# Optimization experiments

Measured on AMD Instinct MI355X. Metric: run time of the kernel, lower is better.

The kernel has to match this reference:

```python
import jax, jax.numpy as jnp
import numpy as np

N, NFEAT, NHID, NCLASS, NHEADS = 50000, 512, 256, 64, 8
C1 = NHID // NHEADS  # 32 per-head channels, layer 1
NEG_SLOPE = 0.2


def setup_inputs() -> dict:
    key = jax.random.key(0)
    ks = jax.random.split(key, 10)
    x = jax.random.normal(ks[0], (N, NFEAT), dtype=jnp.float32)
    edge_idx = jax.random.randint(ks[1], (2, 800000), 0, N, dtype=jnp.int64)
    s = 0.05
    return {
        "x": x,
        "edge_idx": edge_idx,
        "W1": jax.random.normal(ks[2], (NFEAT, NHEADS, C1), dtype=jnp.float32) * s,
        "a1_src": jax.random.normal(ks[3], (NHEADS, C1), dtype=jnp.float32) * s,
        "a1_dst": jax.random.normal(ks[4], (NHEADS, C1), dtype=jnp.float32) * s,
        "b1": jnp.zeros((NHID,), dtype=jnp.float32),
        "W2": jax.random.normal(ks[5], (NHID, NHEADS, NCLASS), dtype=jnp.float32) * s,
        "a2_src": jax.random.normal(ks[6], (NHEADS, NCLASS), dtype=jnp.float32) * s,
        "a2_dst": jax.random.normal(ks[7], (NHEADS, NCLASS), dtype=jnp.float32) * s,
        "b2": jnp.zeros((NCLASS,), dtype=jnp.float32),
    }


def gat_conv(x, src, dst, W, a_src, a_dst, b, concat):
    # x: [N, F_in]; W: [F_in, H, C]; a_*: [H, C]; src/dst: [E]
    h = jnp.einsum("nf,fhc->nhc", x, W)             # [N, H, C]
    e_src = jnp.sum(h * a_src, axis=-1)              # [N, H]
    e_dst = jnp.sum(h * a_dst, axis=-1)              # [N, H]
    alpha = e_src[src] + e_dst[dst]                  # [E, H]
    alpha = jnp.where(alpha > 0, alpha, NEG_SLOPE * alpha)  # leaky_relu(0.2)
    # segment softmax over incoming edges of each destination node
    m = jax.ops.segment_max(alpha, dst, num_segments=N)     # [N, H]
    m = jnp.where(jnp.isfinite(m), m, 0.0)
    e = jnp.exp(alpha - m[dst])                      # [E, H]
    z = jax.ops.segment_sum(e, dst, num_segments=N)  # [N, H]
    coef = e / z[dst]                                # [E, H]
    msg = h[src] * coef[:, :, None]                  # [E, H, C]
    out = jax.ops.segment_sum(msg, dst, num_segments=N)  # [N, H, C]
    if concat:
        out = out.reshape(N, -1)
    else:
        out = out.mean(axis=1)
    return out + b


def reference(x, edge_idx, W1, a1_src, a1_dst, b1, W2, a2_src, a2_dst, b2):
    # add self loops (PyG GATConv default)
    loop = jnp.arange(N, dtype=edge_idx.dtype)
    src = jnp.concatenate([edge_idx[0], loop])
    dst = jnp.concatenate([edge_idx[1], loop])
    h = gat_conv(x, src, dst, W1, a1_src, a1_dst, b1, concat=True)   # [N, NHID]
    h = jax.nn.relu(h)
    # dropout inactive (eval mode)
    out = gat_conv(h, src, dst, W2, a2_src, a2_dst, b2, concat=False)  # [N, NCLASS]
    return jax.nn.log_softmax(out, axis=1)
```

## Files before the change

kernel.cpp:

```cpp
#include <hip/hip_runtime.h>
#include <math.h>

#define NN 50000
#define NF 512
#define NHID 256
#define NCLASS 64
#define NHEADS 8

typedef __attribute__((ext_vector_type(8))) short bf16x8;
typedef __attribute__((ext_vector_type(4))) float f32x4;

static __device__ __forceinline__ unsigned short f2bf(float f) {
  unsigned int u = __float_as_uint(f);
  unsigned int r = (u + 0x7fffu + ((u >> 16) & 1u)) >> 16;
  return (unsigned short)r;
}
static __device__ __forceinline__ float bf2f(unsigned short u) {
  return __uint_as_float(((unsigned int)u) << 16);
}
static __device__ __forceinline__ float2 bfpair(unsigned int u) {
  return make_float2(__uint_as_float(u << 16), __uint_as_float(u & 0xffff0000u));
}

__global__ void k_init_deg(int* deg) {
  int i = blockIdx.x * blockDim.x + threadIdx.x;
  if (i < NN) deg[i] = 1;
}

__global__ void k_count(const int* __restrict__ dst, int E0, int* deg) {
  int i = blockIdx.x * blockDim.x + threadIdx.x;
  if (i < E0) atomicAdd(&deg[dst[i]], 1);
}

__global__ __launch_bounds__(1024) void k_scan(const int* __restrict__ deg, int* offs,
                                               int* cursor) {
  __shared__ int wbase[16];
  __shared__ int srun;
  int tid = threadIdx.x;
  int lane = tid & 63;
  int wv = tid >> 6;
  if (tid == 0) srun = 0;
  __syncthreads();
  for (int base = 0; base < NN; base += 4096) {
    int i = base + tid * 4;
    int4 v;
    if (i + 3 < NN) {
      v = *(const int4*)(deg + i);
    } else {
      v.x = (i + 0 < NN) ? deg[i + 0] : 0;
      v.y = (i + 1 < NN) ? deg[i + 1] : 0;
      v.z = (i + 2 < NN) ? deg[i + 2] : 0;
      v.w = (i + 3 < NN) ? deg[i + 3] : 0;
    }
    int tot = v.x + v.y + v.z + v.w;
    int s = tot;
    #pragma unroll
    for (int o = 1; o < 64; o <<= 1) {
      int t = __shfl_up(s, o);
      if (lane >= o) s += t;
    }
    if (lane == 63) wbase[wv] = s;
    __syncthreads();
    if (tid == 0) {
      int run = srun;
      #pragma unroll
      for (int w2 = 0; w2 < 16; w2++) {
        int t = wbase[w2];
        wbase[w2] = run;
        run += t;
      }
      srun = run;
    }
    __syncthreads();
    int p = wbase[wv] + s - tot;
    if (i + 0 < NN) { offs[i + 0] = p; cursor[i + 0] = p; p += v.x; }
    if (i + 1 < NN) { offs[i + 1] = p; cursor[i + 1] = p; p += v.y; }
    if (i + 2 < NN) { offs[i + 2] = p; cursor[i + 2] = p; p += v.z; }
    if (i + 3 < NN) { offs[i + 3] = p; cursor[i + 3] = p; }
  }
  __syncthreads();
  if (tid == 0) offs[NN] = srun;
}

__global__ void k_scatter(const int* __restrict__ src, const int* __restrict__ dst,
                          int E0, int* cursor, int* __restrict__ nbr) {
  int i = blockIdx.x * blockDim.x + threadIdx.x;
  if (i < E0) {
    int pos = atomicAdd(&cursor[dst[i]], 1);
    nbr[pos] = src[i];
  } else if (i < E0 + NN) {
    int v = i - E0;
    int pos = atomicAdd(&cursor[v], 1);
    nbr[pos] = v;
  }
}

__global__ void k_cast4(const float* __restrict__ in, unsigned short* __restrict__ out,
                        int n4) {
  int i = blockIdx.x * blockDim.x + threadIdx.x;
  if (i >= n4) return;
  float4 v = *(const float4*)(in + (size_t)i * 4);
  ushort4 o;
  o.x = f2bf(v.x); o.y = f2bf(v.y); o.z = f2bf(v.z); o.w = f2bf(v.w);
  *(ushort4*)(out + (size_t)i * 4) = o;
}

__global__ void k_castWt(const float* __restrict__ W, unsigned short* __restrict__ Wt,
                         int K, int cols) {
  int i = blockIdx.x * blockDim.x + threadIdx.x;
  if (i >= K * cols) return;
  int k = i / cols, c = i % cols;
  Wt[(size_t)c * K + k] = f2bf(W[i]);
}

__global__ void k_castWt_perm(const float* __restrict__ W, unsigned short* __restrict__ Wt,
                              int K) {
  int i = blockIdx.x * blockDim.x + threadIdx.x;
  if (i >= K * NHEADS * NCLASS) return;
  int k = i / (NHEADS * NCLASS);
  int rem = i % (NHEADS * NCLASS);
  int h = rem / NCLASS, c = rem % NCLASS;
  Wt[(size_t)(c * NHEADS + h) * K + k] = f2bf(W[i]);
}

__global__ __launch_bounds__(256) void k_gemm_bf(const unsigned short* __restrict__ A,
                                                 const unsigned short* __restrict__ Bt,
                                                 unsigned short* __restrict__ C,
                                                 int rows, int K, int cols) {
  __shared__ unsigned short Bs[256 * 40];
  int t = threadIdx.x;
  int wave = t >> 6, lane = t & 63;
  int quad = lane >> 4, sixt = lane & 15;
  int rb = blockIdx.x * 64 + (wave >> 1) * 32;
  int cw = (wave & 1) * 128;
  int cbw = blockIdx.y * 256 + cw;
  int r0 = rb + sixt, r1 = rb + 16 + sixt;
  const unsigned short* Ap0 = A + (size_t)(r0 < rows ? r0 : 0) * K + quad * 8;
  const unsigned short* Ap1 = A + (size_t)(r1 < rows ? r1 : 0) * K + quad * 8;
  const unsigned short* Bg = Bt + (size_t)(blockIdx.y * 256 + (t >> 2)) * K + (t & 3) * 8;
  const size_t BgStep = (size_t)64 * K;
  char* BsW = (char*)Bs + (t >> 2) * 80 + (t & 3) * 16;
  f32x4 acc0[8] = {}, acc1[8] = {};
  for (int k0 = 0; k0 < K; k0 += 32) {
    uint4 v0 = *(const uint4*)(Bg + k0);
    uint4 v1 = *(const uint4*)(Bg + BgStep + k0);
    uint4 v2 = *(const uint4*)(Bg + 2 * BgStep + k0);
    uint4 v3 = *(const uint4*)(Bg + 3 * BgStep + k0);
    bf16x8 a0 = *(const bf16x8*)(Ap0 + k0);
    bf16x8 a1 = *(const bf16x8*)(Ap1 + k0);
    *(uint4*)(BsW) = v0;
    *(uint4*)(BsW + 64 * 80) = v1;
    *(uint4*)(BsW + 128 * 80) = v2;
    *(uint4*)(BsW + 192 * 80) = v3;
    __syncthreads();
    #pragma unroll
    for (int g = 0; g < 8; g++) {
      bf16x8 b = *(const bf16x8*)((const char*)Bs + (cw + g * 16 + sixt) * 80 + quad * 16);
      acc0[g] = __builtin_amdgcn_mfma_f32_16x16x32_bf16(a0, b, acc0[g], 0, 0, 0);
      acc1[g] = __builtin_amdgcn_mfma_f32_16x16x32_bf16(a1, b, acc1[g], 0, 0, 0);
    }
    __syncthreads();
  }
  #pragma unroll
  for (int r = 0; r < 4; r++) {
    int row = rb + quad * 4 + r;
    if (row < rows) {
      unsigned short* out = C + (size_t)row * cols + cbw + sixt;
      #pragma unroll
      for (int g = 0; g < 8; g++) out[g * 16] = f2bf(acc0[g][r]);
    }
    int row2 = row + 16;
    if (row2 < rows) {
      unsigned short* out = C + (size_t)row2 * cols + cbw + sixt;
      #pragma unroll
      for (int g = 0; g < 8; g++) out[g * 16] = f2bf(acc1[g][r]);
    }
  }
}

template <int C>
__global__ void k_escore_c(const unsigned short* __restrict__ h,
                           const float* __restrict__ asr, const float* __restrict__ ads,
                           float* __restrict__ es, float* __restrict__ ed) {
  int idx = blockIdx.x * blockDim.x + threadIdx.x;
  if (idx >= NN * NHEADS) return;
  int hd = idx & 7;
  const unsigned short* row = h + (size_t)idx * C;
  float s = 0.f, d = 0.f;
  #pragma unroll
  for (int c8 = 0; c8 < C / 8; c8++) {
    uint4 raw = *(const uint4*)(row + c8 * 8);
    float2 p0 = bfpair(raw.x), p1 = bfpair(raw.y), p2 = bfpair(raw.z), p3 = bfpair(raw.w);
    const float* as_ = asr + hd * C + c8 * 8;
    const float* ad_ = ads + hd * C + c8 * 8;
    s += p0.x * as_[0] + p0.y * as_[1] + p1.x * as_[2] + p1.y * as_[3] +
         p2.x * as_[4] + p2.y * as_[5] + p3.x * as_[6] + p3.y * as_[7];
    d += p0.x * ad_[0] + p0.y * ad_[1] + p1.x * ad_[2] + p1.y * ad_[3] +
         p2.x * ad_[4] + p2.y * ad_[5] + p3.x * ad_[6] + p3.y * ad_[7];
  }
  es[idx] = s;
  ed[idx] = d;
}

__global__ void k_escore_p(const unsigned short* __restrict__ h,
                           const float* __restrict__ asr, const float* __restrict__ ads,
                           float* __restrict__ es, float* __restrict__ ed) {
  int idx = blockIdx.x * blockDim.x + threadIdx.x;
  if (idx >= NN * NHEADS) return;
  int hd = idx & 7;
  int n = idx >> 3;
  const unsigned short* row = h + (size_t)n * (NHEADS * NCLASS) + hd;
  float s = 0.f, d = 0.f;
  #pragma unroll
  for (int c = 0; c < NCLASS; c++) {
    float v = bf2f(row[c * NHEADS]);
    s += v * asr[hd * NCLASS + c];
    d += v * ads[hd * NCLASS + c];
  }
  es[idx] = s;
  ed[idx] = d;
}

__global__ __launch_bounds__(256) void k_agg1f(const int* __restrict__ offs,
                                               const int* __restrict__ nbr,
                                               const unsigned short* __restrict__ h1,
                                               const float* __restrict__ es,
                                               const float* __restrict__ ed,
                                               const float* __restrict__ b1,
                                               unsigned short* __restrict__ out) {
  int node = blockIdx.x * 4 + (threadIdx.x >> 6);
  if (node >= NN) return;
  int lane = threadIdx.x & 63;
  int h = lane & 7;
  int beg = offs[node], end = offs[node + 1];
  float edst = ed[node * NHEADS + h];
  float m = -1e30f, z = 0.f;
  for (int k = beg + (lane >> 3); k < end; k += 8) {
    int s = nbr[k];
    float a = es[s * NHEADS + h] + edst;
    a = (a > 0.f) ? a : 0.2f * a;
    float mn = fmaxf(m, a);
    z = z * __expf(m - mn) + __expf(a - mn);
    m = mn;
  }
  #pragma unroll
  for (int o = 8; o < 64; o <<= 1) {
    float m2 = __shfl_xor(m, o);
    float z2 = __shfl_xor(z, o);
    float mn = fmaxf(m, m2);
    z = z * __expf(m - mn) + z2 * __expf(m2 - mn);
    m = mn;
  }
  float inv = 1.f / z;
  int head = lane >> 3;
  float mh = __shfl(m, head);
  float ivh = __shfl(inv, head);
  float edh = __shfl(edst, head);
  float4 acc = make_float4(0.f, 0.f, 0.f, 0.f);
  int k = beg;
  for (; k + 1 < end; k += 2) {
    int s0 = nbr[k], s1 = nbr[k + 1];
    float a0 = es[s0 * NHEADS + head] + edh;
    float a1c = es[s1 * NHEADS + head] + edh;
    a0 = (a0 > 0.f) ? a0 : 0.2f * a0;
    a1c = (a1c > 0.f) ? a1c : 0.2f * a1c;
    float c0 = __expf(a0 - mh) * ivh;
    float c1 = __expf(a1c - mh) * ivh;
    uint2 r0 = *(const uint2*)(h1 + (size_t)s0 * NHID + (lane << 2));
    uint2 r1 = *(const uint2*)(h1 + (size_t)s1 * NHID + (lane << 2));
    float2 p0 = bfpair(r0.x), p1 = bfpair(r0.y);
    float2 q0 = bfpair(r1.x), q1 = bfpair(r1.y);
    acc.x += c0 * p0.x + c1 * q0.x;
    acc.y += c0 * p0.y + c1 * q0.y;
    acc.z += c0 * p1.x + c1 * q1.x;
    acc.w += c0 * p1.y + c1 * q1.y;
  }
  if (k < end) {
    int s0 = nbr[k];
    float a0 = es[s0 * NHEADS + head] + edh;
    a0 = (a0 > 0.f) ? a0 : 0.2f * a0;
    float c0 = __expf(a0 - mh) * ivh;
    uint2 r0 = *(const uint2*)(h1 + (size_t)s0 * NHID + (lane << 2));
    float2 p0 = bfpair(r0.x), p1 = bfpair(r0.y);
    acc.x += c0 * p0.x;
    acc.y += c0 * p0.y;
    acc.z += c0 * p1.x;
    acc.w += c0 * p1.y;
  }
  int col = lane << 2;
  ushort4 o;
  o.x = f2bf(fmaxf(acc.x + b1[col + 0], 0.f));
  o.y = f2bf(fmaxf(acc.y + b1[col + 1], 0.f));
  o.z = f2bf(fmaxf(acc.z + b1[col + 2], 0.f));
  o.w = f2bf(fmaxf(acc.w + b1[col + 3], 0.f));
  *(ushort4*)(out + (size_t)node * NHID + col) = o;
}

__global__ __launch_bounds__(256) void k_agg2f(const int* __restrict__ offs,
                                               const int* __restrict__ nbr,
                                               const unsigned short* __restrict__ h2,
                                               const float* __restrict__ es,
                                               const float* __restrict__ ed,
                                               const float* __restrict__ b2,
                                               float* __restrict__ out) {
  __shared__ float cs[4][64];
  int wv = threadIdx.x >> 6;
  int node = blockIdx.x * 4 + wv;
  if (node >= NN) return;
  int lane = threadIdx.x & 63;
  int h = lane & 7;
  int sub = lane >> 3;
  int beg = offs[node], end = offs[node + 1];
  float edst = ed[node * NHEADS + h];
  float m = -1e30f, z = 0.f;
  for (int k = beg + sub; k < end; k += 8) {
    int s = nbr[k];
    float a = es[s * NHEADS + h] + edst;
    a = (a > 0.f) ? a : 0.2f * a;
    float mn = fmaxf(m, a);
    z = z * __expf(m - mn) + __expf(a - mn);
    m = mn;
  }
  #pragma unroll
  for (int o = 8; o < 64; o <<= 1) {
    float m2 = __shfl_xor(m, o);
    float z2 = __shfl_xor(z, o);
    float mn = fmaxf(m, m2);
    z = z * __expf(m - mn) + z2 * __expf(m2 - mn);
    m = mn;
  }
  float inv = 1.f / z;
  float acc[8] = {};
  for (int kb = beg; kb < end; kb += 8) {
    int ki = kb + sub;
    int s = nbr[ki < end ? ki : end - 1];
    float a = es[s * NHEADS + h] + edst;
    a = (a > 0.f) ? a : 0.2f * a;
    float c = __expf(a - m) * inv;
    cs[wv][sub * 8 + h] = (ki < end) ? c : 0.f;
    int cnt = end - kb;
    if (cnt > 8) cnt = 8;
    for (int e = 0; e < cnt; e++) {
      int se = nbr[kb + e];
      float4 cA = *(const float4*)&cs[wv][e * 8];
      float4 cB = *(const float4*)&cs[wv][e * 8 + 4];
      uint4 r = *(const uint4*)(h2 + (size_t)se * (NHEADS * NCLASS) + (lane << 3));
      float2 p0 = bfpair(r.x), p1 = bfpair(r.y), p2 = bfpair(r.z), p3 = bfpair(r.w);
      acc[0] += cA.x * p0.x;
      acc[1] += cA.y * p0.y;
      acc[2] += cA.z * p1.x;
      acc[3] += cA.w * p1.y;
      acc[4] += cB.x * p2.x;
      acc[5] += cB.y * p2.y;
      acc[6] += cB.z * p3.x;
      acc[7] += cB.w * p3.y;
    }
  }
  float val = 0.f;
  #pragma unroll
  for (int hh = 0; hh < 8; hh++) val += acc[hh];
  val = val * 0.125f + b2[lane];
  float mx = val;
  #pragma unroll
  for (int o = 32; o > 0; o >>= 1) mx = fmaxf(mx, __shfl_xor(mx, o));
  float ex = __expf(val - mx);
  float sm = ex;
  #pragma unroll
  for (int o = 32; o > 0; o >>= 1) sm += __shfl_xor(sm, o);
  out[(size_t)node * NCLASS + lane] = val - mx - __logf(sm);
}

extern "C" void kernel_launch(void* const* d_in, const int* in_sizes, int n_in,
                              void* d_out, int out_size, void* d_ws, size_t ws_size,
                              hipStream_t stream) {
  const float* x   = (const float*)d_in[0];
  const int* eidx  = (const int*)d_in[1];
  const float* W1  = (const float*)d_in[2];
  const float* a1s = (const float*)d_in[3];
  const float* a1d = (const float*)d_in[4];
  const float* b1  = (const float*)d_in[5];
  const float* W2  = (const float*)d_in[6];
  const float* a2s = (const float*)d_in[7];
  const float* a2d = (const float*)d_in[8];
  const float* b2  = (const float*)d_in[9];
  const int E0 = in_sizes[1] / 2;
  const int* esrc = eidx;
  const int* edst = eidx + E0;
  const int E = E0 + NN;

  char* w = (char*)d_ws;
  auto carve = [&](size_t bytes) {
    void* p = (void*)w;
    w += (bytes + 255) & ~(size_t)255;
    return p;
  };
  int* deg      = (int*)carve((size_t)NN * 4);
  int* offs     = (int*)carve((size_t)(NN + 1) * 4);
  int* cursor   = (int*)carve((size_t)NN * 4);
  int* nbr      = (int*)carve((size_t)E * 4);
  float* es1    = (float*)carve((size_t)NN * NHEADS * 4);
  float* ed1    = (float*)carve((size_t)NN * NHEADS * 4);
  unsigned short* xbf   = (unsigned short*)carve((size_t)NN * NF * 2);
  unsigned short* W1t   = (unsigned short*)carve((size_t)NF * NHID * 2);
  unsigned short* W2t   = (unsigned short*)carve((size_t)NHID * NHEADS * NCLASS * 2);
  unsigned short* h1b   = (unsigned short*)carve((size_t)NN * NHID * 2);
  unsigned short* out1b = (unsigned short*)carve((size_t)NN * NHID * 2);
  unsigned short* h2b   = (unsigned short*)carve((size_t)NN * NHEADS * NCLASS * 2);

  k_init_deg<<<(NN + 255) / 256, 256, 0, stream>>>(deg);
  k_count<<<(E0 + 255) / 256, 256, 0, stream>>>(edst, E0, deg);
  k_scan<<<1, 1024, 0, stream>>>(deg, offs, cursor);
  k_scatter<<<(E0 + NN + 255) / 256, 256, 0, stream>>>(esrc, edst, E0, cursor, nbr);

  k_cast4<<<(NN * NF / 4 + 255) / 256, 256, 0, stream>>>(x, xbf, NN * NF / 4);
  k_castWt<<<(NF * NHID + 255) / 256, 256, 0, stream>>>(W1, W1t, NF, NHID);
  k_castWt_perm<<<(NHID * NHEADS * NCLASS + 255) / 256, 256, 0, stream>>>(W2, W2t, NHID);

  k_gemm_bf<<<dim3((NN + 63) / 64, NHID / 256), 256, 0, stream>>>(xbf, W1t, h1b,
                                                                  NN, NF, NHID);
  k_escore_c<32><<<(NN * NHEADS + 255) / 256, 256, 0, stream>>>(h1b, a1s, a1d, es1, ed1);
  k_agg1f<<<(NN + 3) / 4, 256, 0, stream>>>(offs, nbr, h1b, es1, ed1, b1, out1b);

  k_gemm_bf<<<dim3((NN + 63) / 64, (NHEADS * NCLASS) / 256), 256, 0, stream>>>(
      out1b, W2t, h2b, NN, NHID, NHEADS * NCLASS);
  k_escore_p<<<(NN * NHEADS + 255) / 256, 256, 0, stream>>>(h2b, a2s, a2d, es1, ed1);
  k_agg2f<<<(NN + 3) / 4, 256, 0, stream>>>(offs, nbr, h2b, es1, ed1, b2, (float*)d_out);
}
```

Measured before the change: 643.3 us.

## Single-pass online-softmax aggregation with async global-to-LDS neighbor row gathers

Both aggregation kernels drop the separate max/sum pass over incoming edges and use a single-pass online softmax, rescaling the accumulators whenever the running max grows and dividing by z at the end. Neighbor feature rows are gathered eight at a time straight into LDS with global_load_lds, while the next batch's neighbor indices are prefetched and the attention logits computed. The goal is to read the edge list once and overlap the gather latency with the softmax math. The cost is extra rescale work per batch, more LDS per block, and hand-written waitcnt asm whose correctness depends on the compiler's ordering.

```diff
diff --git a/kernel.cpp b/kernel.cpp
--- a/kernel.cpp
+++ b/kernel.cpp
@@ -20,6 +20,11 @@
 }
 static __device__ __forceinline__ float2 bfpair(unsigned int u) {
   return make_float2(__uint_as_float(u << 16), __uint_as_float(u & 0xffff0000u));
+}
+
+static __device__ __forceinline__ void gload16(const void* g, void* l) {
+  __builtin_amdgcn_global_load_lds((const __attribute__((address_space(1))) void*)g,
+                                   (__attribute__((address_space(3))) void*)l, 16, 0, 0);
 }
 
 __global__ void k_init_deg(int* deg) {
@@ -228,71 +233,95 @@
                                                const float* __restrict__ ed,
                                                const float* __restrict__ b1,
                                                unsigned short* __restrict__ out) {
-  int node = blockIdx.x * 4 + (threadIdx.x >> 6);
+  __shared__ __align__(16) unsigned short rows[4][8][256];
+  __shared__ __align__(16) float cs[4][64];
+  int wv = threadIdx.x >> 6;
+  int node = blockIdx.x * 4 + wv;
   if (node >= NN) return;
   int lane = threadIdx.x & 63;
   int h = lane & 7;
+  int sub = lane >> 3;
+  int head = lane >> 3;
+  int col = lane << 2;
   int beg = offs[node], end = offs[node + 1];
   float edst = ed[node * NHEADS + h];
   float m = -1e30f, z = 0.f;
-  for (int k = beg + (lane >> 3); k < end; k += 8) {
-    int s = nbr[k];
-    float a = es[s * NHEADS + h] + edst;
-    a = (a > 0.f) ? a : 0.2f * a;
-    float mn = fmaxf(m, a);
-    z = z * __expf(m - mn) + __expf(a - mn);
+  float4 acc = make_float4(0.f, 0.f, 0.f, 0.f);
+  int kb = beg;
+  int se[8];
+  #pragma unroll
+  for (int e = 0; e < 8; e++) se[e] = nbr[(kb + e < end) ? (kb + e) : kb];
+  int t0 = kb + sub;
+  if (t0 >= end) t0 = end - 1;
+  int sN = nbr[t0];
+  while (true) {
+    int cnt = end - kb;
+    if (cnt > 8) cnt = 8;
+    #pragma unroll
+    for (int e2 = 0; e2 < 4; e2++) {
+      if (2 * e2 < cnt) {
+        int sel = (lane < 32) ? se[2 * e2] : se[2 * e2 + 1];
+        gload16(h1 + (size_t)sel * NHID + (lane & 31) * 8, &rows[wv][2 * e2][0]);
+      }
+    }
+    bool more = (kb + 8 < end);
+    int seN[8];
+    int sNn = 0;
+    if (more) {
+      int kb2 = kb + 8;
+      #pragma unroll
+      for (int e = 0; e < 8; e++) seN[e] = nbr[(kb2 + e < end) ? (kb2 + e) : kb2];
+      int t = kb2 + sub;
+      if (t >= end) t = kb2;
+      sNn = nbr[t];
+    }
+    float a;
+    {
+      float ar = es[(size_t)sN * NHEADS + h] + edst;
+      ar = (ar > 0.f) ? ar : 0.2f * ar;
+      a = (kb + sub < end) ? ar : -1e30f;
+    }
+    float gm = a;
+    #pragma unroll
+    for (int o = 8; o < 64; o <<= 1) gm = fmaxf(gm, __shfl_xor(gm, o));
+    float mn = fmaxf(m, gm);
+    float ee = __expf(a - mn);
+    float zg = ee;
+    #pragma unroll
+    for (int o = 8; o < 64; o <<= 1) zg += __shfl_xor(zg, o);
+    float sc = __expf(m - mn);
+    z = z * sc + zg;
     m = mn;
-  }
-  #pragma unroll
-  for (int o = 8; o < 64; o <<= 1) {
-    float m2 = __shfl_xor(m, o);
-    float z2 = __shfl_xor(z, o);
-    float mn = fmaxf(m, m2);
-    z = z * __expf(m - mn) + z2 * __expf(m2 - mn);
-    m = mn;
+    cs[wv][lane] = ee;
+    asm volatile("s_waitcnt vmcnt(0)" ::: "memory");
+    float sch = __shfl(sc, head);
+    acc.x *= sch; acc.y *= sch; acc.z *= sch; acc.w *= sch;
+    #pragma unroll
+    for (int e = 0; e < 8; e++) {
+      if (e < cnt) {
+        float ce = cs[wv][e * 8 + head];
+        uint2 r = *(const uint2*)&rows[wv][e][lane * 4];
+        float2 p0 = bfpair(r.x), p1 = bfpair(r.y);
+        acc.x += ce * p0.x;
+        acc.y += ce * p0.y;
+        acc.z += ce * p1.x;
+        acc.w += ce * p1.y;
+      }
+    }
+    asm volatile("s_waitcnt lgkmcnt(0)" ::: "memory");
+    if (!more) break;
+    kb += 8;
+    #pragma unroll
+    for (int e = 0; e < 8; e++) se[e] = seN[e];
+    sN = sNn;
   }
   float inv = 1.f / z;
-  int head = lane >> 3;
-  float mh = __shfl(m, head);
   float ivh = __shfl(inv, head);
-  float edh = __shfl(edst, head);
-  float4 acc = make_float4(0.f, 0.f, 0.f, 0.f);
-  int k = beg;
-  for (; k + 1 < end; k += 2) {
-    int s0 = nbr[k], s1 = nbr[k + 1];
-    float a0 = es[s0 * NHEADS + head] + edh;
-    float a1c = es[s1 * NHEADS + head] + edh;
-    a0 = (a0 > 0.f) ? a0 : 0.2f * a0;
-    a1c = (a1c > 0.f) ? a1c : 0.2f * a1c;
-    float c0 = __expf(a0 - mh) * ivh;
-    float c1 = __expf(a1c - mh) * ivh;
-    uint2 r0 = *(const uint2*)(h1 + (size_t)s0 * NHID + (lane << 2));
-    uint2 r1 = *(const uint2*)(h1 + (size_t)s1 * NHID + (lane << 2));
-    float2 p0 = bfpair(r0.x), p1 = bfpair(r0.y);
-    float2 q0 = bfpair(r1.x), q1 = bfpair(r1.y);
-    acc.x += c0 * p0.x + c1 * q0.x;
-    acc.y += c0 * p0.y + c1 * q0.y;
-    acc.z += c0 * p1.x + c1 * q1.x;
-    acc.w += c0 * p1.y + c1 * q1.y;
-  }
-  if (k < end) {
-    int s0 = nbr[k];
-    float a0 = es[s0 * NHEADS + head] + edh;
-    a0 = (a0 > 0.f) ? a0 : 0.2f * a0;
-    float c0 = __expf(a0 - mh) * ivh;
-    uint2 r0 = *(const uint2*)(h1 + (size_t)s0 * NHID + (lane << 2));
-    float2 p0 = bfpair(r0.x), p1 = bfpair(r0.y);
-    acc.x += c0 * p0.x;
-    acc.y += c0 * p0.y;
-    acc.z += c0 * p1.x;
-    acc.w += c0 * p1.y;
-  }
-  int col = lane << 2;
   ushort4 o;
-  o.x = f2bf(fmaxf(acc.x + b1[col + 0], 0.f));
-  o.y = f2bf(fmaxf(acc.y + b1[col + 1], 0.f));
-  o.z = f2bf(fmaxf(acc.z + b1[col + 2], 0.f));
-  o.w = f2bf(fmaxf(acc.w + b1[col + 3], 0.f));
+  o.x = f2bf(fmaxf(acc.x * ivh + b1[col + 0], 0.f));
+  o.y = f2bf(fmaxf(acc.y * ivh + b1[col + 1], 0.f));
+  o.z = f2bf(fmaxf(acc.z * ivh + b1[col + 2], 0.f));
+  o.w = f2bf(fmaxf(acc.w * ivh + b1[col + 3], 0.f));
   *(ushort4*)(out + (size_t)node * NHID + col) = o;
 }
 
@@ -303,7 +332,8 @@
                                                const float* __restrict__ ed,
                                                const float* __restrict__ b2,
                                                float* __restrict__ out) {
-  __shared__ float cs[4][64];
+  __shared__ __align__(16) unsigned short rows[4][8][512];
+  __shared__ __align__(16) float cs[4][64];
   int wv = threadIdx.x >> 6;
   int node = blockIdx.x * 4 + wv;
   if (node >= NN) return;
@@ -313,52 +343,82 @@
   int beg = offs[node], end = offs[node + 1];
   float edst = ed[node * NHEADS + h];
   float m = -1e30f, z = 0.f;
-  for (int k = beg + sub; k < end; k += 8) {
-    int s = nbr[k];
-    float a = es[s * NHEADS + h] + edst;
-    a = (a > 0.f) ? a : 0.2f * a;
-    float mn = fmaxf(m, a);
-    z = z * __expf(m - mn) + __expf(a - mn);
-    m = mn;
-  }
-  #pragma unroll
-  for (int o = 8; o < 64; o <<= 1) {
-    float m2 = __shfl_xor(m, o);
-    float z2 = __shfl_xor(z, o);
-    float mn = fmaxf(m, m2);
-    z = z * __expf(m - mn) + z2 * __expf(m2 - mn);
-    m = mn;
-  }
-  float inv = 1.f / z;
   float acc[8] = {};
-  for (int kb = beg; kb < end; kb += 8) {
-    int ki = kb + sub;
-    int s = nbr[ki < end ? ki : end - 1];
-    float a = es[s * NHEADS + h] + edst;
-    a = (a > 0.f) ? a : 0.2f * a;
-    float c = __expf(a - m) * inv;
-    cs[wv][sub * 8 + h] = (ki < end) ? c : 0.f;
+  int kb = beg;
+  int se[8];
+  #pragma unroll
+  for (int e = 0; e < 8; e++) se[e] = nbr[(kb + e < end) ? (kb + e) : kb];
+  int t0 = kb + sub;
+  if (t0 >= end) t0 = end - 1;
+  int sN = nbr[t0];
+  while (true) {
     int cnt = end - kb;
     if (cnt > 8) cnt = 8;
-    for (int e = 0; e < cnt; e++) {
-      int se = nbr[kb + e];
-      float4 cA = *(const float4*)&cs[wv][e * 8];
-      float4 cB = *(const float4*)&cs[wv][e * 8 + 4];
-      uint4 r = *(const uint4*)(h2 + (size_t)se * (NHEADS * NCLASS) + (lane << 3));
-      float2 p0 = bfpair(r.x), p1 = bfpair(r.y), p2 = bfpair(r.z), p3 = bfpair(r.w);
-      acc[0] += cA.x * p0.x;
-      acc[1] += cA.y * p0.y;
-      acc[2] += cA.z * p1.x;
-      acc[3] += cA.w * p1.y;
-      acc[4] += cB.x * p2.x;
-      acc[5] += cB.y * p2.y;
-      acc[6] += cB.z * p3.x;
-      acc[7] += cB.w * p3.y;
-    }
-  }
+    #pragma unroll
+    for (int e = 0; e < 8; e++) {
+      if (e < cnt)
+        gload16(h2 + (size_t)se[e] * (NHEADS * NCLASS) + lane * 8, &rows[wv][e][0]);
+    }
+    bool more = (kb + 8 < end);
+    int seN[8];
+    int sNn = 0;
+    if (more) {
+      int kb2 = kb + 8;
+      #pragma unroll
+      for (int e = 0; e < 8; e++) seN[e] = nbr[(kb2 + e < end) ? (kb2 + e) : kb2];
+      int t = kb2 + sub;
+      if (t >= end) t = kb2;
+      sNn = nbr[t];
+    }
+    float a;
+    {
+      float ar = es[(size_t)sN * NHEADS + h] + edst;
+      ar = (ar > 0.f) ? ar : 0.2f * ar;
+      a = (kb + sub < end) ? ar : -1e30f;
+    }
+    float gm = a;
+    #pragma unroll
+    for (int o = 8; o < 64; o <<= 1) gm = fmaxf(gm, __shfl_xor(gm, o));
+    float mn = fmaxf(m, gm);
+    float ee = __expf(a - mn);
+    float zg = ee;
+    #pragma unroll
+    for (int o = 8; o < 64; o <<= 1) zg += __shfl_xor(zg, o);
+    float sc = __expf(m - mn);
+    z = z * sc + zg;
+    m = mn;
+    cs[wv][lane] = ee;
+    asm volatile("s_waitcnt vmcnt(0)" ::: "memory");
+    #pragma unroll
+    for (int hh = 0; hh < 8; hh++) acc[hh] *= __shfl(sc, hh);
+    #pragma unroll
+    for (int e = 0; e < 8; e++) {
+      if (e < cnt) {
+        float4 cA = *(const float4*)&cs[wv][e * 8];
+        float4 cB = *(const float4*)&cs[wv][e * 8 + 4];
+        uint4 r = *(const uint4*)&rows[wv][e][lane * 8];
+        float2 p0 = bfpair(r.x), p1 = bfpair(r.y), p2 = bfpair(r.z), p3 = bfpair(r.w);
+        acc[0] += cA.x * p0.x;
+        acc[1] += cA.y * p0.y;
+        acc[2] += cA.z * p1.x;
+        acc[3] += cA.w * p1.y;
+        acc[4] += cB.x * p2.x;
+        acc[5] += cB.y * p2.y;
+        acc[6] += cB.z * p3.x;
+        acc[7] += cB.w * p3.y;
+      }
+    }
+    asm volatile("s_waitcnt lgkmcnt(0)" ::: "memory");
+    if (!more) break;
+    kb += 8;
+    #pragma unroll
+    for (int e = 0; e < 8; e++) se[e] = seN[e];
+    sN = sNn;
+  }
+  float inv = 1.f / z;
   float val = 0.f;
   #pragma unroll
-  for (int hh = 0; hh < 8; hh++) val += acc[hh];
+  for (int hh = 0; hh < 8; hh++) val += acc[hh] * __shfl(inv, hh);
   val = val * 0.125f + b2[lane];
   float mx = val;
   #pragma unroll
```

Result: slower. 714.5 us (+11.1%).
